# Kernel tuning notes

Hardware: AMD Instinct MI355X
Metric: run time of the kernel (lower is better)

## Reference

```python
import jax, jax.numpy as jnp
import numpy as np

B, D, H, W, K = 16, 512, 64, 64, 32


def setup_inputs() -> dict:
    key = jax.random.key(0)
    k1, k2, k3 = jax.random.split(key, 3)
    x = jax.random.normal(k1, (B, D, H, W), dtype=jnp.float32)
    std1 = 1.0 / float(np.sqrt(K * D))
    codewords = jax.random.uniform(k2, (K, D), dtype=jnp.float32, minval=-std1, maxval=std1)
    scale = jax.random.uniform(k3, (K,), dtype=jnp.float32, minval=-1.0, maxval=0.0)
    return {"x": x, "codewords": codewords, "scale": scale}


def reference(x, codewords, scale):
    b, d = x.shape[0], x.shape[1]
    # [b, d, h, w] -> [b, n, d]
    xr = jnp.transpose(x.reshape(b, d, -1), (0, 2, 1))
    # sl[b,n,k] = scale_k^2 * ||x_bn - c_k||^2, expanded to avoid (b,n,k,d) tensor
    x2 = jnp.sum(xr * xr, axis=-1)                      # [b, n]
    c2 = jnp.sum(codewords * codewords, axis=-1)        # [k]
    xc = jnp.einsum('bnd,kd->bnk', xr, codewords)       # [b, n, k]
    sl = (scale * scale)[None, None, :] * (x2[:, :, None] - 2.0 * xc + c2[None, None, :])
    a = jax.nn.softmax(sl, axis=2)                      # softmax over codewords
    # e[b,k,d] = sum_n a[b,n,k] * (x[b,n,d] - c[k,d])
    e = jnp.einsum('bnk,bnd->bkd', a, xr) - jnp.sum(a, axis=1)[:, :, None] * codewords[None]
    return e
```

## Files before the change

kernel.cpp:

```cpp
#include <hip/hip_runtime.h>
#include <hip/hip_fp16.h>

#define BB 16
#define DD 512
#define NN 4096
#define KK 32
#define TNS 32
#define SUBT 4
#define NGRP 32
#define NBLK (BB*NGRP)
#define ROWX 40
#define ROWA 40

#define OFF_XBUF 0
#define OFF_CLDS 40960
#define OFF_AT   73728
#define OFF_X2P  76288
#define OFF_S2   77312
#define OFF_C2   77440
#define OFF_ASUM 77568
#define LDS_TOTAL 77824

typedef unsigned short u16;
typedef __attribute__((ext_vector_type(8))) short short8v;
typedef __attribute__((ext_vector_type(4))) float f32x4;

#define SYNCL() asm volatile("s_waitcnt lgkmcnt(0)\n\ts_barrier" ::: "memory")

__device__ __forceinline__ unsigned f2bf(float f) {
    union { float f; unsigned u; } v; v.f = f;
    unsigned r = v.u + 0x7fff + ((v.u >> 16) & 1);
    return r >> 16;
}

__global__ void k0_prep(const float* __restrict__ cw, const float* __restrict__ scale,
                        u16* __restrict__ c_bf, float* __restrict__ c2,
                        float* __restrict__ s2) {
    const int k = blockIdx.x;
    const int l = threadIdx.x;
    const float* row = cw + k * DD;
    float s = 0.f;
#pragma unroll
    for (int j = 0; j < 8; ++j) {
        float v = row[j * 64 + l];
        s += v * v;
        c_bf[k * DD + j * 64 + l] = (u16)f2bf(v);
    }
#pragma unroll
    for (int off = 32; off; off >>= 1) s += __shfl_xor(s, off);
    if (l == 0) { c2[k] = s; float sc = scale[k]; s2[k] = sc * sc; }
}

template <typename PART>
__global__ __launch_bounds__(512, 4)
void k1_fused(const float* __restrict__ x, const u16* __restrict__ c_bf,
              const float* __restrict__ c2g, const float* __restrict__ s2g,
              float* __restrict__ ws_asum, PART* __restrict__ ws_e) {
    extern __shared__ char smem[];
    u16*   xbuf    = (u16*)(smem + OFF_XBUF);
    u16*   c_lds   = (u16*)(smem + OFF_CLDS);
    u16*   a_t     = (u16*)(smem + OFF_AT);
    float* x2_part = (float*)(smem + OFF_X2P);
    float* s2_l    = (float*)(smem + OFF_S2);
    float* c2_l    = (float*)(smem + OFF_C2);
    float* asum_p  = (float*)(smem + OFF_ASUM);

    const int t = threadIdx.x;
    const int l = t & 63, w = t >> 6;
    const int g = l >> 4, li = l & 15;
    const int blk = blockIdx.x;
    const int b = blk >> 5, grp = blk & 31;
    const int n0 = grp * 128;
    const float* xg = x + (size_t)b * DD * NN + n0;

    const int lr = l >> 3;
    const int lc = l & 7;
    const int cp = lc >> 1, lo = lc & 1;
    const float* xrow = xg + (size_t)(w * 64 + lr) * NN + lc * 4;
    const int wswz = ((cp ^ (lr & 3)) << 4) | (lo << 3);

    float4 va[8];
#pragma unroll
    for (int j = 0; j < 8; ++j) va[j] = *(const float4*)(xrow + (size_t)(j * 8) * NN);

    {
        const int k = t >> 4, seg = t & 15;
#pragma unroll
        for (int j = 0; j < 4; ++j) {
            const int dch = seg * 4 + j;
            short8v v = *(const short8v*)(c_bf + k * DD + dch * 8);
            *(short8v*)(c_lds + k * DD + ((dch ^ (k & 7)) << 3)) = v;
        }
        if (t < KK) { s2_l[t] = s2g[t]; c2_l[t] = c2g[t]; }
    }

    f32x4 accB[8];
#pragma unroll
    for (int dt = 0; dt < 8; ++dt) accB[dt] = (f32x4){0.f, 0.f, 0.f, 0.f};
    float asum_acc[8] = {0.f, 0.f, 0.f, 0.f, 0.f, 0.f, 0.f, 0.f};

#pragma unroll
    for (int s = 0; s < SUBT; ++s) {
        {
            float p0 = 0, p1 = 0, p2 = 0, p3 = 0;
#pragma unroll
            for (int j = 0; j < 8; ++j) {
                uint2 pk;
                asm("v_cvt_pk_bf16_f32 %0, %1, %2" : "=v"(pk.x) : "v"(va[j].x), "v"(va[j].y));
                asm("v_cvt_pk_bf16_f32 %0, %1, %2" : "=v"(pk.y) : "v"(va[j].z), "v"(va[j].w));
                const int r = w * 64 + j * 8 + lr;
                *(uint2*)(smem + OFF_XBUF + r * 80 + wswz) = pk;
                p0 += va[j].x * va[j].x; p1 += va[j].y * va[j].y;
                p2 += va[j].z * va[j].z; p3 += va[j].w * va[j].w;
            }
            p0 += __shfl_xor(p0, 8); p0 += __shfl_xor(p0, 16); p0 += __shfl_xor(p0, 32);
            p1 += __shfl_xor(p1, 8); p1 += __shfl_xor(p1, 16); p1 += __shfl_xor(p1, 32);
            p2 += __shfl_xor(p2, 8); p2 += __shfl_xor(p2, 16); p2 += __shfl_xor(p2, 32);
            p3 += __shfl_xor(p3, 8); p3 += __shfl_xor(p3, 16); p3 += __shfl_xor(p3, 32);
            if (lr == 0) {
                float4 p4 = {p0, p1, p2, p3};
                *(float4*)((char*)smem + OFF_X2P + w * 128 + lc * 16) = p4;
            }
        }
        SYNCL();

        if (s < SUBT - 1) {
#pragma unroll
            for (int j = 0; j < 8; ++j)
                va[j] = *(const float4*)(xrow + (size_t)(j * 8) * NN + (s + 1) * TNS);
        }

        if (w < 2) {
            f32x4 accA0 = {0.f, 0.f, 0.f, 0.f}, accA1 = {0.f, 0.f, 0.f, 0.f};
            const int nloc = w * 16 + li;
            const int nc = nloc >> 3, nr = nloc & 7;
            for (int ch = 0; ch < 16; ++ch) {
                const int dbase = ch * 32 + g * 8;
                short8v bf;
#pragma unroll
                for (int j = 0; j < 8; ++j) {
                    const int d = dbase + j;
                    bf[j] = (short)xbuf[d * ROWX + ((nc ^ (d & 3)) << 3) + nr];
                }
                const int csw = ((ch * 4 + g) ^ (li & 7)) << 3;
                short8v a0 = *(const short8v*)(c_lds + li * DD + csw);
                short8v a1 = *(const short8v*)(c_lds + (16 + li) * DD + csw);
                accA0 = __builtin_amdgcn_mfma_f32_16x16x32_bf16(a0, bf, accA0, 0, 0, 0);
                accA1 = __builtin_amdgcn_mfma_f32_16x16x32_bf16(a1, bf, accA1, 0, 0, 0);
            }
            float x2v = 0.f;
#pragma unroll
            for (int p = 0; p < 8; ++p) x2v += x2_part[p * 32 + nloc];
            float sl[8];
            float mx = -3.4e38f;
#pragma unroll
            for (int r = 0; r < 4; ++r) {
                float v0 = s2_l[4 * g + r]      * (x2v - 2.f * accA0[r] + c2_l[4 * g + r]);
                float v1 = s2_l[16 + 4 * g + r] * (x2v - 2.f * accA1[r] + c2_l[16 + 4 * g + r]);
                sl[r] = v0; sl[4 + r] = v1;
                mx = fmaxf(mx, fmaxf(v0, v1));
            }
            mx = fmaxf(mx, __shfl_xor(mx, 16));
            mx = fmaxf(mx, __shfl_xor(mx, 32));
            float sum = 0.f;
#pragma unroll
            for (int i = 0; i < 8; ++i) { sl[i] = __expf(sl[i] - mx); sum += sl[i]; }
            sum += __shfl_xor(sum, 16);
            sum += __shfl_xor(sum, 32);
            const float inv = 1.f / sum;
#pragma unroll
            for (int i = 0; i < 8; ++i) {
                float a = sl[i] * inv;
                int k = (i < 4) ? (4 * g + i) : (16 + 4 * g + (i - 4));
                a_t[k * ROWA + nloc] = (u16)f2bf(a);
                float ssum = a;
                ssum += __shfl_xor(ssum, 1); ssum += __shfl_xor(ssum, 2);
                ssum += __shfl_xor(ssum, 4); ssum += __shfl_xor(ssum, 8);
                asum_acc[i] += ssum;
            }
        }
        SYNCL();

        {
            const int kt = w >> 2, dblk = w & 3;
            short8v af = *(const short8v*)(a_t + (kt * 16 + li) * ROWA + g * 8);
#pragma unroll
            for (int dt = 0; dt < 8; ++dt) {
                const int d = dblk * 128 + dt * 16 + li;
                short8v xf = *(const short8v*)(xbuf + d * ROWX + ((g ^ (d & 3)) << 3));
                accB[dt] = __builtin_amdgcn_mfma_f32_16x16x32_bf16(af, xf, accB[dt], 0, 0, 0);
            }
        }
        SYNCL();
    }

    if (w < 2 && li == 0) {
#pragma unroll
        for (int i = 0; i < 8; ++i) {
            int k = (i < 4) ? (4 * g + i) : (16 + 4 * g + (i - 4));
            asum_p[w * KK + k] = asum_acc[i];
        }
    }
    __syncthreads();
    if (t < KK) ws_asum[(size_t)blk * KK + t] = asum_p[t] + asum_p[KK + t];

    {
        const int kt = w >> 2, dblk = w & 3;
        const size_t ebase = (size_t)blk * KK * DD;
#pragma unroll
        for (int dt = 0; dt < 8; ++dt)
#pragma unroll
            for (int r = 0; r < 4; ++r) {
                int k = kt * 16 + 4 * g + r;
                int d = dblk * 128 + dt * 16 + li;
                ws_e[ebase + (size_t)k * DD + d] = (PART)(accB[dt][r]);
            }
    }
}

__global__ void k2_reduce_h(const __half2* __restrict__ ws_e, const float* __restrict__ ws_asum,
                            const float* __restrict__ cw, float* __restrict__ out) {
    int tid = blockIdx.x * blockDim.x + threadIdx.x;
    int d2 = tid & 255;
    int k = (tid >> 8) & (KK - 1);
    int b = tid >> 13;
    const __half2* pe = ws_e + ((size_t)(b * NGRP) * KK + k) * 256 + d2;
    const float* pa = ws_asum + b * NGRP * KK + k;
    float s0 = 0.f, s1 = 0.f, as = 0.f;
#pragma unroll
    for (int tl = 0; tl < NGRP; ++tl) {
        float2 f = __half22float2(pe[(size_t)tl * KK * 256]);
        s0 += f.x; s1 += f.y;
        as += pa[tl * KK];
    }
    int d = d2 * 2;
    float c0 = cw[k * DD + d], c1 = cw[k * DD + d + 1];
    float2 o; o.x = s0 - as * c0; o.y = s1 - as * c1;
    *(float2*)(out + ((size_t)(b * KK + k) * DD + d)) = o;
}

__global__ void k2_reduce_f(const float* __restrict__ ws_e, const float* __restrict__ ws_asum,
                            const float* __restrict__ cw, float* __restrict__ out) {
    int tid = blockIdx.x * blockDim.x + threadIdx.x;
    int d = tid & (DD - 1);
    int k = (tid >> 9) & (KK - 1);
    int b = tid >> 14;
    float s = 0.f, as = 0.f;
#pragma unroll
    for (int tl = 0; tl < NGRP; ++tl) {
        int blk = b * NGRP + tl;
        s += ws_e[((size_t)blk * KK + k) * DD + d];
        as += ws_asum[(size_t)blk * KK + k];
    }
    out[tid] = s - as * cw[k * DD + d];
}

extern "C" void kernel_launch(void* const* d_in, const int* in_sizes, int n_in,
                              void* d_out, int out_size, void* d_ws, size_t ws_size,
                              hipStream_t stream) {
    const float* x = (const float*)d_in[0];
    const float* cw = (const float*)d_in[1];
    const float* scale = (const float*)d_in[2];
    float* out = (float*)d_out;

    char* ws = (char*)d_ws;
    u16*   c_bf    = (u16*)ws;
    float* c2      = (float*)(ws + 32768);
    float* s2      = (float*)(ws + 32896);
    float* ws_asum = (float*)(ws + 33024);
    char*  e_ptr   = ws + 98560;

    const size_t need_h = 98560 + (size_t)NBLK * KK * DD * sizeof(__half);

    k0_prep<<<KK, 64, 0, stream>>>(cw, scale, c_bf, c2, s2);
    if (ws_size >= need_h) {
        k1_fused<__half><<<NBLK, 512, LDS_TOTAL, stream>>>(x, c_bf, c2, s2, ws_asum, (__half*)e_ptr);
        k2_reduce_h<<<(BB * KK * 256) / 256, 256, 0, stream>>>((const __half2*)e_ptr, ws_asum, cw, out);
    } else {
        k1_fused<float><<<NBLK, 512, LDS_TOTAL, stream>>>(x, c_bf, c2, s2, ws_asum, (float*)e_ptr);
        k2_reduce_f<<<(BB * KK * DD) / 256, 256, 0, stream>>>((const float*)e_ptr, ws_asum, cw, out);
    }
}
```

Baseline: 43.95 us.

## Fold codeword prep into fused kernel, split x prefetch, raise softmax wave priority

```diff
diff --git a/kernel.cpp b/kernel.cpp
--- a/kernel.cpp
+++ b/kernel.cpp
@@ -33,28 +33,10 @@
     return r >> 16;
 }
 
-__global__ void k0_prep(const float* __restrict__ cw, const float* __restrict__ scale,
-                        u16* __restrict__ c_bf, float* __restrict__ c2,
-                        float* __restrict__ s2) {
-    const int k = blockIdx.x;
-    const int l = threadIdx.x;
-    const float* row = cw + k * DD;
-    float s = 0.f;
-#pragma unroll
-    for (int j = 0; j < 8; ++j) {
-        float v = row[j * 64 + l];
-        s += v * v;
-        c_bf[k * DD + j * 64 + l] = (u16)f2bf(v);
-    }
-#pragma unroll
-    for (int off = 32; off; off >>= 1) s += __shfl_xor(s, off);
-    if (l == 0) { c2[k] = s; float sc = scale[k]; s2[k] = sc * sc; }
-}
-
 template <typename PART>
 __global__ __launch_bounds__(512, 4)
-void k1_fused(const float* __restrict__ x, const u16* __restrict__ c_bf,
-              const float* __restrict__ c2g, const float* __restrict__ s2g,
+void k1_fused(const float* __restrict__ x, const float* __restrict__ cw,
+              const float* __restrict__ scale,
               float* __restrict__ ws_asum, PART* __restrict__ ws_e) {
     extern __shared__ char smem[];
     u16*   xbuf    = (u16*)(smem + OFF_XBUF);
@@ -79,19 +61,40 @@
     const float* xrow = xg + (size_t)(w * 64 + lr) * NN + lc * 4;
     const int wswz = ((cp ^ (lr & 3)) << 4) | (lo << 3);
 
-    float4 va[8];
-#pragma unroll
-    for (int j = 0; j < 8; ++j) va[j] = *(const float4*)(xrow + (size_t)(j * 8) * NN);
-
+    const int ck = t >> 4, cseg = t & 15;
+    float4 cv[8];
     {
-        const int k = t >> 4, seg = t & 15;
+        const float* crow = cw + ck * DD + cseg * 32;
+#pragma unroll
+        for (int j = 0; j < 8; ++j) cv[j] = *(const float4*)(crow + 4 * j);
+    }
+
+    float4 vaA[4], vaB[4];
+#pragma unroll
+    for (int j = 0; j < 4; ++j) vaA[j] = *(const float4*)(xrow + (size_t)(j * 8) * NN);
+#pragma unroll
+    for (int j = 0; j < 4; ++j) vaB[j] = *(const float4*)(xrow + (size_t)((j + 4) * 8) * NN);
+
+    {
+        float c2p = 0.f;
+#pragma unroll
+        for (int j = 0; j < 8; ++j)
+            c2p += cv[j].x * cv[j].x + cv[j].y * cv[j].y
+                 + cv[j].z * cv[j].z + cv[j].w * cv[j].w;
 #pragma unroll
         for (int j = 0; j < 4; ++j) {
-            const int dch = seg * 4 + j;
-            short8v v = *(const short8v*)(c_bf + k * DD + dch * 8);
-            *(short8v*)(c_lds + k * DD + ((dch ^ (k & 7)) << 3)) = v;
-        }
-        if (t < KK) { s2_l[t] = s2g[t]; c2_l[t] = c2g[t]; }
+            uint4 pk;
+            asm("v_cvt_pk_bf16_f32 %0, %1, %2" : "=v"(pk.x) : "v"(cv[2*j].x),   "v"(cv[2*j].y));
+            asm("v_cvt_pk_bf16_f32 %0, %1, %2" : "=v"(pk.y) : "v"(cv[2*j].z),   "v"(cv[2*j].w));
+            asm("v_cvt_pk_bf16_f32 %0, %1, %2" : "=v"(pk.z) : "v"(cv[2*j+1].x), "v"(cv[2*j+1].y));
+            asm("v_cvt_pk_bf16_f32 %0, %1, %2" : "=v"(pk.w) : "v"(cv[2*j+1].z), "v"(cv[2*j+1].w));
+            const int dch = cseg * 4 + j;
+            *(uint4*)(smem + OFF_CLDS + ck * 1024 + ((dch ^ (ck & 7)) << 4)) = pk;
+        }
+        c2p += __shfl_xor(c2p, 1); c2p += __shfl_xor(c2p, 2);
+        c2p += __shfl_xor(c2p, 4); c2p += __shfl_xor(c2p, 8);
+        if ((l & 15) == 0) c2_l[ck] = c2p;
+        if (t < KK) { float sc = scale[t]; s2_l[t] = sc * sc; }
     }
 
     f32x4 accB[8];
@@ -105,13 +108,14 @@
             float p0 = 0, p1 = 0, p2 = 0, p3 = 0;
 #pragma unroll
             for (int j = 0; j < 8; ++j) {
+                float4 v = (j < 4) ? vaA[j] : vaB[j - 4];
                 uint2 pk;
-                asm("v_cvt_pk_bf16_f32 %0, %1, %2" : "=v"(pk.x) : "v"(va[j].x), "v"(va[j].y));
-                asm("v_cvt_pk_bf16_f32 %0, %1, %2" : "=v"(pk.y) : "v"(va[j].z), "v"(va[j].w));
+                asm("v_cvt_pk_bf16_f32 %0, %1, %2" : "=v"(pk.x) : "v"(v.x), "v"(v.y));
+                asm("v_cvt_pk_bf16_f32 %0, %1, %2" : "=v"(pk.y) : "v"(v.z), "v"(v.w));
                 const int r = w * 64 + j * 8 + lr;
                 *(uint2*)(smem + OFF_XBUF + r * 80 + wswz) = pk;
-                p0 += va[j].x * va[j].x; p1 += va[j].y * va[j].y;
-                p2 += va[j].z * va[j].z; p3 += va[j].w * va[j].w;
+                p0 += v.x * v.x; p1 += v.y * v.y;
+                p2 += v.z * v.z; p3 += v.w * v.w;
             }
             p0 += __shfl_xor(p0, 8); p0 += __shfl_xor(p0, 16); p0 += __shfl_xor(p0, 32);
             p1 += __shfl_xor(p1, 8); p1 += __shfl_xor(p1, 16); p1 += __shfl_xor(p1, 32);
@@ -126,11 +130,12 @@
 
         if (s < SUBT - 1) {
 #pragma unroll
-            for (int j = 0; j < 8; ++j)
-                va[j] = *(const float4*)(xrow + (size_t)(j * 8) * NN + (s + 1) * TNS);
+            for (int j = 0; j < 4; ++j)
+                vaA[j] = *(const float4*)(xrow + (size_t)(j * 8) * NN + (s + 1) * TNS);
         }
 
         if (w < 2) {
+            __builtin_amdgcn_s_setprio(1);
             f32x4 accA0 = {0.f, 0.f, 0.f, 0.f}, accA1 = {0.f, 0.f, 0.f, 0.f};
             const int nloc = w * 16 + li;
             const int nc = nloc >> 3, nr = nloc & 7;
@@ -178,6 +183,13 @@
                 ssum += __shfl_xor(ssum, 4); ssum += __shfl_xor(ssum, 8);
                 asum_acc[i] += ssum;
             }
+            __builtin_amdgcn_s_setprio(0);
+        }
+
+        if (s < SUBT - 1) {
+#pragma unroll
+            for (int j = 0; j < 4; ++j)
+                vaB[j] = *(const float4*)(xrow + (size_t)((j + 4) * 8) * NN + (s + 1) * TNS);
         }
         SYNCL();
 
@@ -264,20 +276,16 @@
     float* out = (float*)d_out;
 
     char* ws = (char*)d_ws;
-    u16*   c_bf    = (u16*)ws;
-    float* c2      = (float*)(ws + 32768);
-    float* s2      = (float*)(ws + 32896);
-    float* ws_asum = (float*)(ws + 33024);
-    char*  e_ptr   = ws + 98560;
-
-    const size_t need_h = 98560 + (size_t)NBLK * KK * DD * sizeof(__half);
-
-    k0_prep<<<KK, 64, 0, stream>>>(cw, scale, c_bf, c2, s2);
+    float* ws_asum = (float*)ws;
+    char*  e_ptr   = ws + 65536;
+
+    const size_t need_h = 65536 + (size_t)NBLK * KK * DD * sizeof(__half);
+
     if (ws_size >= need_h) {
-        k1_fused<__half><<<NBLK, 512, LDS_TOTAL, stream>>>(x, c_bf, c2, s2, ws_asum, (__half*)e_ptr);
+        k1_fused<__half><<<NBLK, 512, LDS_TOTAL, stream>>>(x, cw, scale, ws_asum, (__half*)e_ptr);
         k2_reduce_h<<<(BB * KK * 256) / 256, 256, 0, stream>>>((const __half2*)e_ptr, ws_asum, cw, out);
     } else {
-        k1_fused<float><<<NBLK, 512, LDS_TOTAL, stream>>>(x, c_bf, c2, s2, ws_asum, (float*)e_ptr);
+        k1_fused<float><<<NBLK, 512, LDS_TOTAL, stream>>>(x, cw, scale, ws_asum, (float*)e_ptr);
         k2_reduce_f<<<(BB * KK * DD) / 256, 256, 0, stream>>>((const float*)e_ptr, ws_asum, cw, out);
     }
 }
```

Measured after the change: 38.44 us. -12.5%, faster.
